# Performance work log

Hardware: AMD Instinct MI355X
Metric: run time of the kernel (lower is better)

Reference implementation:

```python
import jax, jax.numpy as jnp
import numpy as np

LN_EPS = 1e-5
BOUNDARY_ID = 0  # boundary_ids = {space_id} = {0}


def setup_inputs() -> dict:
    key = jax.random.key(0)
    k1, k2, k3 = jax.random.split(key, 3)
    B, T, D = 16, 8192, 256
    x = jax.random.normal(k1, (B, T, D), dtype=jnp.float32)
    input_ids = jax.random.randint(k2, (B, T), 0, 8, dtype=jnp.int64)
    W_proj = jax.random.normal(k3, (D, D), dtype=jnp.float32) / np.sqrt(D)
    b_proj = jnp.zeros((D,), dtype=jnp.float32)
    gamma = jnp.ones((D,), dtype=jnp.float32)
    beta = jnp.zeros((D,), dtype=jnp.float32)
    return {"x": x, "input_ids": input_ids, "W_proj": W_proj,
            "b_proj": b_proj, "gamma": gamma, "beta": beta}


def _pool(x, input_ids):
    # Boundary-defined segment mean pooling, vectorized via segment_sum.
    B, T, D = x.shape
    boundary = input_ids == BOUNDARY_ID                       # [B,T]
    nonb = ~boundary
    # A segment starts at a non-boundary token at t=0 or right after a boundary.
    prev_is_b = jnp.concatenate(
        [jnp.ones((B, 1), dtype=bool), boundary[:, :-1]], axis=1)
    start = nonb & prev_is_b
    seg = jnp.cumsum(start.astype(jnp.int32), axis=1) - 1     # seg idx per token
    MAXW = T  # static upper bound on number of segments (jit-safe padding)
    row_off = jnp.arange(B, dtype=jnp.int32)[:, None] * MAXW
    dump = B * MAXW  # boundary tokens go to a dummy segment, dropped below
    flat_ids = jnp.where(nonb, seg + row_off, dump).reshape(-1)
    sums = jax.ops.segment_sum(x.reshape(-1, D), flat_ids,
                               num_segments=B * MAXW + 1)[:-1]
    counts = jax.ops.segment_sum(jnp.ones((B * T,), x.dtype), flat_ids,
                                 num_segments=B * MAXW + 1)[:-1]
    sums = sums.reshape(B, MAXW, D)
    counts = counts.reshape(B, MAXW)
    mask = (counts > 0).astype(x.dtype)                       # [B,MAXW]
    padded = sums / jnp.maximum(counts, 1.0)[..., None]       # zeros where empty
    return padded, mask


def reference(x, input_ids, W_proj, b_proj, gamma, beta):
    padded, mask = _pool(x, input_ids)
    out = jnp.einsum('bwd,ed->bwe', padded, W_proj) + b_proj  # nn.Linear
    mu = jnp.mean(out, axis=-1, keepdims=True)
    var = jnp.mean(jnp.square(out - mu), axis=-1, keepdims=True)
    out = (out - mu) * jax.lax.rsqrt(var + LN_EPS) * gamma + beta
    return out, mask
```

## Files before the change

### kernel.cpp

```cpp
#include <hip/hip_runtime.h>
#include <hip/hip_bf16.h>
#include <math.h>

#define BB 16
#define TT 8192
#define DD 256
#define MAXSEG 4096
#define RPB 8
#define LN_EPS 1e-5f

__device__ inline float4 f4add(float4 a, float4 b) {
    a.x += b.x; a.y += b.y; a.z += b.z; a.w += b.w; return a;
}

__global__ __launch_bounds__(1024) void setup_kernel(
    const int* __restrict__ ids, const float* __restrict__ W,
    const float* __restrict__ bp, const float* __restrict__ gamma,
    const float* __restrict__ beta, int* __restrict__ counts,
    int* __restrict__ seg_start, int* __restrict__ nseg_g,
    float* __restrict__ mask_out, float* __restrict__ Wt,
    float* __restrict__ ln_empty) {
    __shared__ int wtot_s[16];
    __shared__ int wtot_n[16];
    __shared__ int segs[MAXSEG];
    __shared__ int pvals[MAXSEG];

    int tid = threadIdx.x;
    int lane = tid & 63;
    int wv = tid >> 6;

    if (blockIdx.x >= BB) {
        int bi = blockIdx.x - BB;
        if (bi < 64) {
            int d = bi * 4 + (tid >> 8);
            int e = tid & 255;
            Wt[d * DD + e] = W[e * DD + d];
        } else if (wv == 0) {
            int e0 = lane * 4;
            float4 v = *(const float4*)(bp + e0);
            float s = v.x + v.y + v.z + v.w;
            float sq = v.x * v.x + v.y * v.y + v.z * v.z + v.w * v.w;
#pragma unroll
            for (int o = 32; o > 0; o >>= 1) {
                s += __shfl_down(s, o);
                sq += __shfl_down(sq, o);
            }
            s = __shfl(s, 0);
            sq = __shfl(sq, 0);
            float mu = s * (1.f / (float)DD);
            float var = sq * (1.f / (float)DD) - mu * mu;
            float rs = rsqrtf(fmaxf(var, 0.f) + LN_EPS);
            float4 ge = *(const float4*)(gamma + e0);
            float4 be = *(const float4*)(beta + e0);
            float4 o4;
            o4.x = (v.x - mu) * rs * ge.x + be.x;
            o4.y = (v.y - mu) * rs * ge.y + be.y;
            o4.z = (v.z - mu) * rs * ge.z + be.z;
            o4.w = (v.w - mu) * rs * ge.w + be.w;
            *(float4*)(ln_empty + e0) = o4;
        }
        return;
    }

    const int TPT = 8;
    int b = blockIdx.x;
    const int* row = ids + b * TT;
    int t0 = tid * TPT;

    int4 q0 = ((const int4*)(row + t0))[0];
    int4 q1 = ((const int4*)(row + t0))[1];
    int v[TPT] = {q0.x, q0.y, q0.z, q0.w, q1.x, q1.y, q1.z, q1.w};
    int prev = (tid == 0) ? 0 : row[t0 - 1];

    bool nb[TPT], st[TPT];
    int cstart = 0, cnon = 0;
#pragma unroll
    for (int j = 0; j < TPT; ++j) {
        nb[j] = (v[j] != 0);
        int pv = (j == 0) ? prev : v[j - 1];
        st[j] = nb[j] && (pv == 0);
        cstart += st[j] ? 1 : 0;
        cnon += nb[j] ? 1 : 0;
    }

    int ss = cstart, sn = cnon;
#pragma unroll
    for (int o = 1; o < 64; o <<= 1) {
        int us = __shfl_up(ss, o);
        int un = __shfl_up(sn, o);
        if (lane >= o) { ss += us; sn += un; }
    }
    if (lane == 63) { wtot_s[wv] = ss; wtot_n[wv] = sn; }
    __syncthreads();

    int bs = 0, bn = 0, tot_s = 0, tot_n = 0;
#pragma unroll
    for (int j = 0; j < 16; ++j) {
        int a = wtot_s[j], c = wtot_n[j];
        if (j < wv) { bs += a; bn += c; }
        tot_s += a; tot_n += c;
    }
    bs += ss - cstart;
    bn += sn - cnon;

#pragma unroll
    for (int j = 0; j < TPT; ++j) {
        if (st[j]) { segs[bs] = t0 + j; pvals[bs] = bn; bs++; }
        bn += nb[j] ? 1 : 0;
    }
    __syncthreads();

    int ns = tot_s;
    for (int w = tid; w < TT; w += 1024) {
        int c = 0;
        if (w < ns) {
            int pe = (w + 1 < ns) ? pvals[w + 1] : tot_n;
            c = pe - pvals[w];
            seg_start[b * TT + w] = segs[w];
        }
        counts[b * TT + w] = c;
        mask_out[b * TT + w] = (w < ns) ? 1.0f : 0.0f;
    }
    if (tid == 0) nseg_g[b] = ns;
}

__global__ __launch_bounds__(128) void pool_gemm_ln(
    const float* __restrict__ x, const float* __restrict__ Wt,
    const float* __restrict__ bp, const float* __restrict__ gamma,
    const float* __restrict__ beta, const int* __restrict__ counts,
    const int* __restrict__ seg_start, const int* __restrict__ nseg,
    const float* __restrict__ ln_e, float* __restrict__ out) {
    __shared__ float pooled[RPB][DD];
    __shared__ float red[2][RPB][2];

    int b = blockIdx.x;
    int wbase = blockIdx.y * RPB;
    int ns = nseg[b];
    int tid = threadIdx.x;
    int lane = tid & 63;
    int wv = tid >> 6;
    size_t rowbase = ((size_t)(b * TT + wbase)) * DD;

    if (wbase >= ns) {
        float4 lv = *(const float4*)(ln_e + 4 * lane);
        float* o = out + rowbase + (size_t)(wv * 4) * DD + 4 * lane;
#pragma unroll
        for (int r = 0; r < 4; ++r)
            *(float4*)(o + (size_t)r * DD) = lv;
        return;
    }
    int nr = min(RPB, ns - wbase);

#pragma unroll
    for (int r = 0; r < 4; ++r) {
        int row = wv * 4 + r;
        float4 a0 = {0, 0, 0, 0};
        if (row < nr) {
            int w = wbase + row;
            int s = seg_start[b * TT + w];
            int len = counts[b * TT + w];
            const float4* xp = (const float4*)(x + ((size_t)(b * TT + s)) * DD) + lane;
            float4 a1 = a0, a2 = a0, a3 = a0;
            int t = 0;
            for (; t + 4 <= len; t += 4) {
                a0 = f4add(a0, xp[(t + 0) * 64]);
                a1 = f4add(a1, xp[(t + 1) * 64]);
                a2 = f4add(a2, xp[(t + 2) * 64]);
                a3 = f4add(a3, xp[(t + 3) * 64]);
            }
            for (; t < len; ++t) a0 = f4add(a0, xp[t * 64]);
            a0 = f4add(f4add(a0, a1), f4add(a2, a3));
            float inv = 1.f / (float)len;
            a0.x *= inv; a0.y *= inv; a0.z *= inv; a0.w *= inv;
        }
        *(float4*)&pooled[row][lane * 4] = a0;
    }
    __syncthreads();

    int c0 = wv * 128 + lane * 2;
    float2 acc[RPB];
    float2 bias2 = *(const float2*)(bp + c0);
#pragma unroll
    for (int r = 0; r < RPB; ++r) acc[r] = bias2;

    const float* Wc = Wt + c0;
    float2 w0 = *(const float2*)(Wc + 0 * DD);
    float2 w1 = *(const float2*)(Wc + 1 * DD);
    float2 w2 = *(const float2*)(Wc + 2 * DD);
    float2 w3 = *(const float2*)(Wc + 3 * DD);
#pragma unroll 1
    for (int d0 = 0; d0 < DD; d0 += 4) {
        int dn = (d0 + 4) & 255;
        float2 n0 = *(const float2*)(Wc + (dn + 0) * DD);
        float2 n1 = *(const float2*)(Wc + (dn + 1) * DD);
        float2 n2 = *(const float2*)(Wc + (dn + 2) * DD);
        float2 n3 = *(const float2*)(Wc + (dn + 3) * DD);
#pragma unroll
        for (int r = 0; r < RPB; ++r) {
            const float4 p = *(const float4*)&pooled[r][d0];
            acc[r].x = fmaf(p.x, w0.x, acc[r].x);
            acc[r].y = fmaf(p.x, w0.y, acc[r].y);
            acc[r].x = fmaf(p.y, w1.x, acc[r].x);
            acc[r].y = fmaf(p.y, w1.y, acc[r].y);
            acc[r].x = fmaf(p.z, w2.x, acc[r].x);
            acc[r].y = fmaf(p.z, w2.y, acc[r].y);
            acc[r].x = fmaf(p.w, w3.x, acc[r].x);
            acc[r].y = fmaf(p.w, w3.y, acc[r].y);
        }
        w0 = n0; w1 = n1; w2 = n2; w3 = n3;
    }

#pragma unroll
    for (int r = 0; r < RPB; ++r) {
        float s = acc[r].x + acc[r].y;
        float sq = acc[r].x * acc[r].x + acc[r].y * acc[r].y;
#pragma unroll
        for (int o = 32; o > 0; o >>= 1) {
            s += __shfl_down(s, o);
            sq += __shfl_down(sq, o);
        }
        if (lane == 0) { red[wv][r][0] = s; red[wv][r][1] = sq; }
    }
    __syncthreads();

    float ga0 = gamma[c0], ga1 = gamma[c0 + 1];
    float be0 = beta[c0], be1 = beta[c0 + 1];
#pragma unroll
    for (int r = 0; r < RPB; ++r) {
        float s = red[0][r][0] + red[1][r][0];
        float sq = red[0][r][1] + red[1][r][1];
        float mu = s * (1.f / (float)DD);
        float var = sq * (1.f / (float)DD) - mu * mu;
        float rs = rsqrtf(fmaxf(var, 0.f) + LN_EPS);
        float2 v;
        v.x = (acc[r].x - mu) * rs * ga0 + be0;
        v.y = (acc[r].y - mu) * rs * ga1 + be1;
        *(float2*)(out + rowbase + (size_t)r * DD + c0) = v;
    }
}

extern "C" void kernel_launch(void* const* d_in, const int* in_sizes, int n_in,
                              void* d_out, int out_size, void* d_ws, size_t ws_size,
                              hipStream_t stream) {
    const float* x = (const float*)d_in[0];
    const int* ids = (const int*)d_in[1];
    const float* W = (const float*)d_in[2];
    const float* bp = (const float*)d_in[3];
    const float* gamma = (const float*)d_in[4];
    const float* beta = (const float*)d_in[5];

    float* out = (float*)d_out;
    float* mask = out + (size_t)BB * TT * DD;

    char* ws = (char*)d_ws;
    int* counts = (int*)ws;
    int* seg_start = (int*)(ws + (size_t)BB * TT * 4);
    int* nseg = (int*)(ws + (size_t)2 * BB * TT * 4);
    float* Wt = (float*)(ws + (size_t)2 * BB * TT * 4 + 256);
    float* ln_e = Wt + DD * DD;

    hipLaunchKernelGGL(setup_kernel, dim3(BB + 64 + 1), dim3(1024), 0, stream,
                       ids, W, bp, gamma, beta, counts, seg_start, nseg, mask,
                       Wt, ln_e);
    hipLaunchKernelGGL(pool_gemm_ln, dim3(BB, TT / RPB), dim3(128), 0, stream,
                       x, Wt, bp, gamma, beta, counts, seg_start, nseg, ln_e, out);
}
```

Baseline: 281.3 us.

## Split empty-row fill into separate kernel and widen work blocks to 256 threads

Moves the LayerNorm-of-bias fill for empty segment rows out of the pooling/GEMM kernel into its own fill kernel. The work kernel is widened to 256 threads, with each thread owning one output column and each wave pooling two rows. Output writes switch to nontemporal stores. The goal is more parallelism per block, less divergence between empty and full blocks, and less cache pollution from the large output stream. The cost is an extra kernel launch and a second full grid of mostly early-exit blocks.

```diff
diff --git a/kernel.cpp b/kernel.cpp
--- a/kernel.cpp
+++ b/kernel.cpp
@@ -8,6 +8,8 @@
 #define MAXSEG 4096
 #define RPB 8
 #define LN_EPS 1e-5f
+
+typedef float vfloat4 __attribute__((ext_vector_type(4)));
 
 __device__ inline float4 f4add(float4 a, float4 b) {
     a.x += b.x; a.y += b.y; a.z += b.z; a.w += b.w; return a;
@@ -124,36 +126,27 @@
     if (tid == 0) nseg_g[b] = ns;
 }
 
-__global__ __launch_bounds__(128) void pool_gemm_ln(
+__global__ __launch_bounds__(256) void work_kernel(
     const float* __restrict__ x, const float* __restrict__ Wt,
     const float* __restrict__ bp, const float* __restrict__ gamma,
     const float* __restrict__ beta, const int* __restrict__ counts,
     const int* __restrict__ seg_start, const int* __restrict__ nseg,
-    const float* __restrict__ ln_e, float* __restrict__ out) {
+    float* __restrict__ out) {
     __shared__ float pooled[RPB][DD];
-    __shared__ float red[2][RPB][2];
+    __shared__ float red[4][RPB][2];
 
     int b = blockIdx.x;
     int wbase = blockIdx.y * RPB;
     int ns = nseg[b];
+    if (wbase >= ns) return;
+    int nr = min(RPB, ns - wbase);
     int tid = threadIdx.x;
     int lane = tid & 63;
     int wv = tid >> 6;
-    size_t rowbase = ((size_t)(b * TT + wbase)) * DD;
-
-    if (wbase >= ns) {
-        float4 lv = *(const float4*)(ln_e + 4 * lane);
-        float* o = out + rowbase + (size_t)(wv * 4) * DD + 4 * lane;
-#pragma unroll
-        for (int r = 0; r < 4; ++r)
-            *(float4*)(o + (size_t)r * DD) = lv;
-        return;
-    }
-    int nr = min(RPB, ns - wbase);
-
-#pragma unroll
-    for (int r = 0; r < 4; ++r) {
-        int row = wv * 4 + r;
+
+#pragma unroll
+    for (int rr = 0; rr < 2; ++rr) {
+        int row = wv * 2 + rr;
         float4 a0 = {0, 0, 0, 0};
         if (row < nr) {
             int w = wbase + row;
@@ -177,43 +170,39 @@
     }
     __syncthreads();
 
-    int c0 = wv * 128 + lane * 2;
-    float2 acc[RPB];
-    float2 bias2 = *(const float2*)(bp + c0);
-#pragma unroll
-    for (int r = 0; r < RPB; ++r) acc[r] = bias2;
-
-    const float* Wc = Wt + c0;
-    float2 w0 = *(const float2*)(Wc + 0 * DD);
-    float2 w1 = *(const float2*)(Wc + 1 * DD);
-    float2 w2 = *(const float2*)(Wc + 2 * DD);
-    float2 w3 = *(const float2*)(Wc + 3 * DD);
+    int c = wv * 64 + lane;
+    float acc[RPB];
+    float bias = bp[c];
+#pragma unroll
+    for (int r = 0; r < RPB; ++r) acc[r] = bias;
+
+    const float* Wc = Wt + c;
+    float w0 = Wc[0 * DD];
+    float w1 = Wc[1 * DD];
+    float w2 = Wc[2 * DD];
+    float w3 = Wc[3 * DD];
 #pragma unroll 1
     for (int d0 = 0; d0 < DD; d0 += 4) {
         int dn = (d0 + 4) & 255;
-        float2 n0 = *(const float2*)(Wc + (dn + 0) * DD);
-        float2 n1 = *(const float2*)(Wc + (dn + 1) * DD);
-        float2 n2 = *(const float2*)(Wc + (dn + 2) * DD);
-        float2 n3 = *(const float2*)(Wc + (dn + 3) * DD);
+        float n0 = Wc[(dn + 0) * DD];
+        float n1 = Wc[(dn + 1) * DD];
+        float n2 = Wc[(dn + 2) * DD];
+        float n3 = Wc[(dn + 3) * DD];
 #pragma unroll
         for (int r = 0; r < RPB; ++r) {
             const float4 p = *(const float4*)&pooled[r][d0];
-            acc[r].x = fmaf(p.x, w0.x, acc[r].x);
-            acc[r].y = fmaf(p.x, w0.y, acc[r].y);
-            acc[r].x = fmaf(p.y, w1.x, acc[r].x);
-            acc[r].y = fmaf(p.y, w1.y, acc[r].y);
-            acc[r].x = fmaf(p.z, w2.x, acc[r].x);
-            acc[r].y = fmaf(p.z, w2.y, acc[r].y);
-            acc[r].x = fmaf(p.w, w3.x, acc[r].x);
-            acc[r].y = fmaf(p.w, w3.y, acc[r].y);
+            acc[r] = fmaf(p.x, w0, acc[r]);
+            acc[r] = fmaf(p.y, w1, acc[r]);
+            acc[r] = fmaf(p.z, w2, acc[r]);
+            acc[r] = fmaf(p.w, w3, acc[r]);
         }
         w0 = n0; w1 = n1; w2 = n2; w3 = n3;
     }
 
 #pragma unroll
     for (int r = 0; r < RPB; ++r) {
-        float s = acc[r].x + acc[r].y;
-        float sq = acc[r].x * acc[r].x + acc[r].y * acc[r].y;
+        float s = acc[r];
+        float sq = acc[r] * acc[r];
 #pragma unroll
         for (int o = 32; o > 0; o >>= 1) {
             s += __shfl_down(s, o);
@@ -223,19 +212,35 @@
     }
     __syncthreads();
 
-    float ga0 = gamma[c0], ga1 = gamma[c0 + 1];
-    float be0 = beta[c0], be1 = beta[c0 + 1];
+    size_t rowbase = ((size_t)(b * TT + wbase)) * DD;
+    float ga = gamma[c], be = beta[c];
 #pragma unroll
     for (int r = 0; r < RPB; ++r) {
-        float s = red[0][r][0] + red[1][r][0];
-        float sq = red[0][r][1] + red[1][r][1];
+        float s = red[0][r][0] + red[1][r][0] + red[2][r][0] + red[3][r][0];
+        float sq = red[0][r][1] + red[1][r][1] + red[2][r][1] + red[3][r][1];
         float mu = s * (1.f / (float)DD);
         float var = sq * (1.f / (float)DD) - mu * mu;
         float rs = rsqrtf(fmaxf(var, 0.f) + LN_EPS);
-        float2 v;
-        v.x = (acc[r].x - mu) * rs * ga0 + be0;
-        v.y = (acc[r].y - mu) * rs * ga1 + be1;
-        *(float2*)(out + rowbase + (size_t)r * DD + c0) = v;
+        float v = (acc[r] - mu) * rs * ga + be;
+        __builtin_nontemporal_store(v, out + rowbase + (size_t)r * DD + c);
+    }
+}
+
+__global__ __launch_bounds__(256) void fill_kernel(const int* __restrict__ nseg,
+                                                   const float* __restrict__ ln_e,
+                                                   float* __restrict__ out) {
+    int b = blockIdx.x;
+    int wbase = blockIdx.y * RPB;
+    if (wbase < nseg[b]) return;
+    int tid = threadIdx.x;
+    int lane = tid & 63;
+    int wv = tid >> 6;
+    vfloat4 lv = *(const vfloat4*)(ln_e + 4 * lane);
+    float* o = out + ((size_t)(b * TT + wbase)) * DD + 4 * lane;
+#pragma unroll
+    for (int rr = 0; rr < 2; ++rr) {
+        int row = wv * 2 + rr;
+        __builtin_nontemporal_store(lv, (vfloat4*)(o + (size_t)row * DD));
     }
 }
 
@@ -262,6 +267,8 @@
     hipLaunchKernelGGL(setup_kernel, dim3(BB + 64 + 1), dim3(1024), 0, stream,
                        ids, W, bp, gamma, beta, counts, seg_start, nseg, mask,
                        Wt, ln_e);
-    hipLaunchKernelGGL(pool_gemm_ln, dim3(BB, TT / RPB), dim3(128), 0, stream,
-                       x, Wt, bp, gamma, beta, counts, seg_start, nseg, ln_e, out);
-}
+    hipLaunchKernelGGL(work_kernel, dim3(BB, TT / RPB), dim3(256), 0, stream,
+                       x, Wt, bp, gamma, beta, counts, seg_start, nseg, out);
+    hipLaunchKernelGGL(fill_kernel, dim3(BB, TT / RPB), dim3(256), 0, stream,
+                       nseg, ln_e, out);
+}
```

Result: slower. 290.0 us (+3.1%).
